# Kernel optimization log

Measured on AMD Instinct MI355X. Metric: run time of the kernel, lower is better.

Reference implementation:

```python
import jax, jax.numpy as jnp
import numpy as np
import math

B, T, E, H = 4, 2048, 1024, 16
D = E // H

def setup_inputs() -> dict:
    key = jax.random.key(0)
    k1, k2, k3 = jax.random.split(key, 3)
    x = jax.random.normal(k1, (B, T, E), dtype=jnp.float32)
    # GPT-2 Conv1D: out = x @ W + b, W shape [in, out]
    W_attn = jax.random.normal(k2, (E, 3 * E), dtype=jnp.float32) * 0.02
    b_attn = jnp.zeros((3 * E,), dtype=jnp.float32)
    W_proj = jax.random.normal(k3, (E, E), dtype=jnp.float32) * 0.02
    b_proj = jnp.zeros((E,), dtype=jnp.float32)
    # causal mask, broadcastable [1,1,T,T]; masked where mask == 0
    mask = jnp.tril(jnp.ones((T, T), dtype=jnp.int32))[None, None]
    return {"x": x, "mask": mask, "W_attn": W_attn, "b_attn": b_attn,
            "W_proj": W_proj, "b_proj": b_proj}

def reference(x, mask, W_attn, b_attn, W_proj, b_proj):
    Bx, Tx, Ex = x.shape
    qkv = x @ W_attn + b_attn                      # [B,T,3E]
    q, k, v = jnp.split(qkv, 3, axis=-1)
    q = q.reshape(Bx, Tx, H, D)
    k = k.reshape(Bx, Tx, H, D)
    v = v.reshape(Bx, Tx, H, D)
    att = jnp.einsum('bqhd,bkhd->bhqk', q, k) / math.sqrt(D)
    att = jnp.where(mask == 0, jnp.float32(-1e20), att)
    att = jax.nn.softmax(att, axis=-1)
    y = jnp.einsum('bhqk,bkhd->bqhd', att, v).reshape(Bx, Tx, Ex)
    y = y @ W_proj + b_proj
    return y
```

## Files before the change

### kernel.cpp

```cpp
#include <hip/hip_runtime.h>
#include <hip/hip_bf16.h>

#define BB 4
#define TT 2048
#define EE 1024
#define HH 16
#define DD 64
#define PART_SZ (BB*HH*TT*DD)

typedef __bf16 bf16x8_t __attribute__((ext_vector_type(8)));
typedef float floatx4_t __attribute__((ext_vector_type(4)));

__device__ __forceinline__ unsigned short f2bf(float f) {
    union { float f; unsigned int i; } v; v.f = f;
    unsigned int x = v.i;
    return (unsigned short)((x + 0x7FFFu + ((x >> 16) & 1u)) >> 16);
}
__device__ __forceinline__ unsigned int pack2(float lo, float hi) {
    return (unsigned int)f2bf(lo) | ((unsigned int)f2bf(hi) << 16);
}
__device__ __forceinline__ unsigned int cvt_pk_bf16(float lo, float hi) {
    unsigned int r;
    asm("v_cvt_pk_bf16_f32 %0, %1, %2" : "=v"(r) : "v"(lo), "v"(hi));
    return r;
}

typedef __attribute__((address_space(1))) const unsigned int gu32_t;
typedef __attribute__((address_space(3))) unsigned int lu32_t;
__device__ __forceinline__ void gl_lds16(const unsigned short* g, unsigned short* l) {
    __builtin_amdgcn_global_load_lds((gu32_t*)g, (lu32_t*)l, 16, 0, 0);
}

__global__ __launch_bounds__(256)
void cvt_x_k(const float* __restrict__ x, unsigned short* __restrict__ xb)
{
    const size_t i = ((size_t)blockIdx.x * 256 + threadIdx.x) * 8;
    float4 a = *(const float4*)(x + i);
    float4 b = *(const float4*)(x + i + 4);
    uint4 p;
    p.x = pack2(a.x, a.y); p.y = pack2(a.z, a.w);
    p.z = pack2(b.x, b.y); p.w = pack2(b.z, b.w);
    *(uint4*)(xb + i) = p;
}

__global__ __launch_bounds__(256)
void transpose_w_k(const float* __restrict__ W, unsigned short* __restrict__ WT, int N)
{
    __shared__ unsigned short L[64 * 72];
    const int tid = threadIdx.x;
    const int tn = blockIdx.x * 64;
    const int tk = blockIdx.y * 64;
    {
        const int k  = tid >> 2;
        const int n0 = (tid & 3) * 16;
        const float* src = W + (size_t)(tk + k) * N + tn + n0;
        float4 f0 = *(const float4*)(src);
        float4 f1 = *(const float4*)(src + 4);
        float4 f2 = *(const float4*)(src + 8);
        float4 f3 = *(const float4*)(src + 12);
        uint4 p0, p1;
        p0.x = pack2(f0.x, f0.y); p0.y = pack2(f0.z, f0.w);
        p0.z = pack2(f1.x, f1.y); p0.w = pack2(f1.z, f1.w);
        p1.x = pack2(f2.x, f2.y); p1.y = pack2(f2.z, f2.w);
        p1.z = pack2(f3.x, f3.y); p1.w = pack2(f3.z, f3.w);
        *(uint4*)(&L[k * 72 + n0])     = p0;
        *(uint4*)(&L[k * 72 + n0 + 8]) = p1;
    }
    __syncthreads();
    {
        const int n  = tid >> 2;
        const int k0 = (tid & 3) * 16;
        unsigned short u[16];
        #pragma unroll
        for (int e = 0; e < 16; e++) u[e] = L[(k0 + e) * 72 + n];
        unsigned short* dst = WT + (size_t)(tn + n) * 1024 + tk + k0;
        *(uint4*)(dst)     = *(uint4*)&u[0];
        *(uint4*)(dst + 8) = *(uint4*)&u[8];
    }
}

template<int MODE>
__global__ __launch_bounds__(256, 2)
void gemm_k(const unsigned short* __restrict__ Ag,
            const unsigned short* __restrict__ Wt,
            const float* __restrict__ biasg,
            unsigned short* __restrict__ Qo,
            unsigned short* __restrict__ Ko,
            unsigned short* __restrict__ Vo,
            float* __restrict__ Fo)
{
    constexpr int N = (MODE == 0) ? 3072 : 1024;
    __shared__ unsigned short Al[128 * 32];
    __shared__ unsigned short Bl[128 * 32];
    constexpr size_t EPSZ = (MODE == 0) ? (4 * 16 * 72 * 2) : (4 * 16 * 68 * 4);
    __shared__ __align__(16) char EpRaw[EPSZ];
    const int tid  = threadIdx.x;
    int bn, bm;
    if (MODE == 0) {
        const int id = blockIdx.x;
        const int s  = id & 7;
        const int t  = id >> 3;
        const int P  = (t / 12) * 8 + s;
        bm = (P >> 1) * 128;
        bn = ((P & 1) * 12 + (t % 12)) * 128;
    } else {
        const int id = blockIdx.x;
        const int s  = id & 7;
        const int t  = id >> 3;
        bm = ((t & 7) * 8 + s) * 128;
        bn = (t >> 3) * 128;
    }
    const int lane = tid & 63;
    const int wv   = tid >> 6;
    const int wm   = (wv & 1) * 64;
    const int wn   = (wv >> 1) * 64;
    const int l16  = lane & 15;
    const int quad = lane >> 4;
    const int lrow = lane >> 2;
    const int lk   = (lane & 3) * 8;

    const bool flip = (MODE == 1) || (bn < 2 * EE);

    floatx4_t acc[4][4];
    #pragma unroll
    for (int i = 0; i < 4; i++)
        #pragma unroll
        for (int j = 0; j < 4; j++)
            acc[i][j] = (floatx4_t){0.f, 0.f, 0.f, 0.f};

    for (int k0 = 0; k0 < 1024; k0 += 32) {
        __syncthreads();
        #pragma unroll
        for (int t = 0; t < 2; t++) {
            const int rb = wv * 32 + t * 16;
            gl_lds16(Ag + (size_t)(bm + rb + lrow) * 1024 + k0 + lk, &Al[rb * 32]);
            gl_lds16(Wt + (size_t)(bn + rb + lrow) * 1024 + k0 + lk, &Bl[rb * 32]);
        }
        __syncthreads();

        bf16x8_t af[4], bfr[4];
        #pragma unroll
        for (int i = 0; i < 4; i++)
            af[i]  = *(const bf16x8_t*)(&Al[(wm + i * 16 + l16) * 32 + quad * 8]);
        #pragma unroll
        for (int j = 0; j < 4; j++)
            bfr[j] = *(const bf16x8_t*)(&Bl[(wn + j * 16 + l16) * 32 + quad * 8]);
        if (flip) {
            #pragma unroll
            for (int u = 0; u < 4; u++)
                #pragma unroll
                for (int v = 0; v < 4; v++)
                    acc[u][v] = __builtin_amdgcn_mfma_f32_16x16x32_bf16(bfr[u], af[v], acc[u][v], 0, 0, 0);
        } else {
            #pragma unroll
            for (int u = 0; u < 4; u++)
                #pragma unroll
                for (int v = 0; v < 4; v++)
                    acc[u][v] = __builtin_amdgcn_mfma_f32_16x16x32_bf16(af[u], bfr[v], acc[u][v], 0, 0, 0);
        }
    }

    const int rdrow = lane >> 2;
    const int rdseg = (lane & 3) * 16;

    if (MODE == 1) {
        float* Epf = (float*)EpRaw + wv * 16 * 68;
        floatx4_t bv[4];
        #pragma unroll
        for (int u = 0; u < 4; u++)
            bv[u] = *(const floatx4_t*)(biasg + bn + wn + u * 16 + quad * 4);
        #pragma unroll
        for (int v = 0; v < 4; v++) {
            #pragma unroll
            for (int u = 0; u < 4; u++) {
                floatx4_t val;
                #pragma unroll
                for (int rr = 0; rr < 4; rr++) val[rr] = acc[u][v][rr] + bv[u][rr];
                *(floatx4_t*)(&Epf[l16 * 68 + u * 16 + quad * 4]) = val;
            }
            __builtin_amdgcn_s_waitcnt(0);
            const int m = bm + wm + v * 16 + rdrow;
            float* dst = Fo + (size_t)m * N + bn + wn + rdseg;
            const float* srcl = &Epf[rdrow * 68 + rdseg];
            #pragma unroll
            for (int c = 0; c < 4; c++)
                *(floatx4_t*)(dst + c * 4) = *(const floatx4_t*)(srcl + c * 4);
        }
    } else if (flip) {
        unsigned short* Ep = (unsigned short*)EpRaw + wv * 16 * 72;
        floatx4_t bv[4];
        #pragma unroll
        for (int u = 0; u < 4; u++)
            bv[u] = *(const floatx4_t*)(biasg + bn + wn + u * 16 + quad * 4);
        const int p  = bn >> 10;
        const int h  = ((bn + wn) & 1023) >> 6;
        const int d0 = rdseg & 63;
        unsigned short* outb = (p == 0) ? Qo : Ko;
        #pragma unroll
        for (int v = 0; v < 4; v++) {
            #pragma unroll
            for (int u = 0; u < 4; u++) {
                uint2 pk;
                pk.x = pack2(acc[u][v][0] + bv[u][0], acc[u][v][1] + bv[u][1]);
                pk.y = pack2(acc[u][v][2] + bv[u][2], acc[u][v][3] + bv[u][3]);
                *(uint2*)(&Ep[l16 * 72 + u * 16 + quad * 4]) = pk;
            }
            __builtin_amdgcn_s_waitcnt(0);
            const int t  = bm + wm + v * 16 + rdrow;
            const int b_ = t >> 11, t_ = t & 2047;
            unsigned short* dst = outb + ((size_t)(b_ * HH + h) * TT + t_) * DD + d0;
            const unsigned short* srcl = &Ep[rdrow * 72 + rdseg];
            *(uint4*)(dst)     = *(const uint4*)(srcl);
            *(uint4*)(dst + 8) = *(const uint4*)(srcl + 8);
        }
    } else {
        unsigned short* Ep = (unsigned short*)EpRaw + wv * 16 * 72;
        #pragma unroll
        for (int v = 0; v < 4; v++) {
            const float bias_v = biasg[bn + wn + v * 16 + l16];
            #pragma unroll
            for (int u = 0; u < 4; u++) {
                uint2 pk;
                pk.x = pack2(acc[u][v][0] + bias_v, acc[u][v][1] + bias_v);
                pk.y = pack2(acc[u][v][2] + bias_v, acc[u][v][3] + bias_v);
                *(uint2*)(&Ep[l16 * 72 + u * 16 + quad * 4]) = pk;
            }
            __builtin_amdgcn_s_waitcnt(0);
            const int n  = bn + wn + v * 16 + rdrow;
            const int h  = (n & 1023) >> 6, d = n & 63;
            const int t0 = bm + wm + rdseg;
            const int b_ = t0 >> 11, t_ = t0 & 2047;
            unsigned short* dst = Vo + ((size_t)(b_ * HH + h) * DD + d) * TT + t_;
            const unsigned short* srcl = &Ep[rdrow * 72 + rdseg];
            *(uint4*)(dst)     = *(const uint4*)(srcl);
            *(uint4*)(dst + 8) = *(const uint4*)(srcl + 8);
        }
    }
}

__global__ __launch_bounds__(256, 4)
void attn_k(const unsigned short* __restrict__ Qg,
            const unsigned short* __restrict__ Kg,
            const unsigned short* __restrict__ Vg,
            unsigned short* __restrict__ Og)
{
    __shared__ unsigned short Kt[64 * 72];
    __shared__ unsigned short Vt[64 * 72];
    __shared__ unsigned short Pw[4][16 * 72];
    const int tid  = threadIdx.x;
    const int w    = tid >> 6;
    const int lane = tid & 63;
    const int l16  = lane & 15;
    const int quad = lane >> 4;
    const int id = blockIdx.x;
    const int qt = 31 - ((id >> 3) & 31);
    const int bh = (id & 7) + 8 * (id >> 8);
    const int qb   = qt * 64;
    const int qw   = qb + w * 16;
    const size_t base = (size_t)bh * TT * DD;
    const float C = 0.18033688f;

    bf16x8_t qf[2];
    #pragma unroll
    for (int ks = 0; ks < 2; ks++)
        qf[ks] = *(const bf16x8_t*)(Qg + base + (size_t)(qw + l16) * DD + ks * 32 + quad * 8);

    floatx4_t oacc[4];
    #pragma unroll
    for (int n = 0; n < 4; n++) oacc[n] = (floatx4_t){0.f, 0.f, 0.f, 0.f};
    float lacc = 0.f;

    const int kend = qb + 64;
    const int srow = tid >> 2;
    const int sc0  = (tid & 3) * 16;
    const int qq   = qw + l16;
    const int kqb  = quad * 4;
    for (int kb = 0; kb < kend; kb += 64) {
        __syncthreads();
        {
            const unsigned short* kg = Kg + base + (size_t)(kb + srow) * DD + sc0;
            uint4 ka = *(const uint4*)(kg);
            uint4 kb2 = *(const uint4*)(kg + 8);
            *(uint4*)(&Kt[srow * 72 + sc0])     = ka;
            *(uint4*)(&Kt[srow * 72 + sc0 + 8]) = kb2;
            const unsigned short* vg = Vg + base + (size_t)srow * TT + kb + sc0;
            uint4 va = *(const uint4*)(vg);
            uint4 vb = *(const uint4*)(vg + 8);
            *(uint4*)(&Vt[srow * 72 + sc0])     = va;
            *(uint4*)(&Vt[srow * 72 + sc0 + 8]) = vb;
        }
        __syncthreads();
        if (kb < qw + 16) {
            floatx4_t sacc[4];
            #pragma unroll
            for (int n = 0; n < 4; n++) sacc[n] = (floatx4_t){0.f, 0.f, 0.f, 0.f};
            #pragma unroll
            for (int n = 0; n < 4; n++) {
                #pragma unroll
                for (int ks = 0; ks < 2; ks++) {
                    bf16x8_t kf = *(const bf16x8_t*)(&Kt[(n * 16 + l16) * 72 + ks * 32 + quad * 8]);
                    sacc[n] = __builtin_amdgcn_mfma_f32_16x16x32_bf16(kf, qf[ks], sacc[n], 0, 0, 0);
                }
            }
            if ((kb + 63) > qw) {
                #pragma unroll
                for (int n = 0; n < 4; n++) {
                    const int keyb = kb + n * 16 + kqb;
                    #pragma unroll
                    for (int rr = 0; rr < 4; rr++)
                        if (keyb + rr > qq) sacc[n][rr] = -1e30f;
                }
            }
            #pragma unroll
            for (int n = 0; n < 4; n++) {
                const float p0 = __builtin_exp2f(sacc[n][0] * C);
                const float p1 = __builtin_exp2f(sacc[n][1] * C);
                const float p2 = __builtin_exp2f(sacc[n][2] * C);
                const float p3 = __builtin_exp2f(sacc[n][3] * C);
                lacc += (p0 + p1) + (p2 + p3);
                uint2 pk;
                pk.x = cvt_pk_bf16(p0, p1);
                pk.y = cvt_pk_bf16(p2, p3);
                *(uint2*)(&Pw[w][l16 * 72 + n * 16 + kqb]) = pk;
            }
            bf16x8_t pf[2];
            #pragma unroll
            for (int ks = 0; ks < 2; ks++)
                pf[ks] = *(const bf16x8_t*)(&Pw[w][l16 * 72 + ks * 32 + quad * 8]);
            #pragma unroll
            for (int n = 0; n < 4; n++) {
                #pragma unroll
                for (int ks = 0; ks < 2; ks++) {
                    bf16x8_t vf = *(const bf16x8_t*)(&Vt[(n * 16 + l16) * 72 + ks * 32 + quad * 8]);
                    oacc[n] = __builtin_amdgcn_mfma_f32_16x16x32_bf16(pf[ks], vf, oacc[n], 0, 0, 0);
                }
            }
        }
    }
    float lsum = lacc;
    lsum += __shfl_xor(lsum, 16);
    lsum += __shfl_xor(lsum, 32);
    const float inv = 1.f / lsum;
    const int b_ = bh >> 4, h_ = bh & 15;
    #pragma unroll
    for (int rr = 0; rr < 4; rr++) {
        const float invr = __int_as_float(
            __builtin_amdgcn_ds_bpermute((quad * 4 + rr) * 4, __float_as_int(inv)));
        const int q = qw + quad * 4 + rr;
        unsigned short* op = Og + (((size_t)b_ * TT + q) * HH + h_) * DD;
        #pragma unroll
        for (int n = 0; n < 4; n++)
            op[n * 16 + l16] = f2bf(oacc[n][rr] * invr);
    }
}

extern "C" void kernel_launch(void* const* d_in, const int* in_sizes, int n_in,
                              void* d_out, int out_size, void* d_ws, size_t ws_size,
                              hipStream_t stream) {
    const float* x      = (const float*)d_in[0];
    const float* W_attn = (const float*)d_in[2];
    const float* b_attn = (const float*)d_in[3];
    const float* W_proj = (const float*)d_in[4];
    const float* b_proj = (const float*)d_in[5];
    float* out = (float*)d_out;

    unsigned short* Qs  = (unsigned short*)d_out;
    unsigned short* Ks  = Qs + (size_t)PART_SZ;
    unsigned short* VTs = (unsigned short*)d_ws;
    unsigned short* Ao  = VTs + (size_t)PART_SZ;
    unsigned short* Xb  = Ao + (size_t)PART_SZ;
    unsigned short* WaT = Xb + (size_t)PART_SZ;
    unsigned short* WpT = WaT + (size_t)3072 * 1024;

    cvt_x_k<<<PART_SZ / (256 * 8), 256, 0, stream>>>(x, Xb);
    transpose_w_k<<<dim3(48, 16), 256, 0, stream>>>(W_attn, WaT, 3072);
    transpose_w_k<<<dim3(16, 16), 256, 0, stream>>>(W_proj, WpT, 1024);

    gemm_k<0><<<1536, 256, 0, stream>>>(Xb, WaT, b_attn, Qs, Ks, VTs, nullptr);

    attn_k<<<2048, 256, 0, stream>>>(Qs, Ks, VTs, Ao);

    gemm_k<1><<<512, 256, 0, stream>>>(Ao, WpT, b_proj, nullptr, nullptr, nullptr, out);
}
```

Baseline: 305.2 us.

## Pair causal query tiles per block to share K/V loads; prescale Q

Measured after the change: 287.0 us. -6.0%, faster.

```diff
diff --git a/kernel.cpp b/kernel.cpp
--- a/kernel.cpp
+++ b/kernel.cpp
@@ -196,13 +196,14 @@
         const int h  = ((bn + wn) & 1023) >> 6;
         const int d0 = rdseg & 63;
         unsigned short* outb = (p == 0) ? Qo : Ko;
+        const float sc = (p == 0) ? 0.18033688f : 1.0f;
         #pragma unroll
         for (int v = 0; v < 4; v++) {
             #pragma unroll
             for (int u = 0; u < 4; u++) {
                 uint2 pk;
-                pk.x = pack2(acc[u][v][0] + bv[u][0], acc[u][v][1] + bv[u][1]);
-                pk.y = pack2(acc[u][v][2] + bv[u][2], acc[u][v][3] + bv[u][3]);
+                pk.x = pack2((acc[u][v][0] + bv[u][0]) * sc, (acc[u][v][1] + bv[u][1]) * sc);
+                pk.y = pack2((acc[u][v][2] + bv[u][2]) * sc, (acc[u][v][3] + bv[u][3]) * sc);
                 *(uint2*)(&Ep[l16 * 72 + u * 16 + quad * 4]) = pk;
             }
             __builtin_amdgcn_s_waitcnt(0);
@@ -253,28 +254,86 @@
     const int l16  = lane & 15;
     const int quad = lane >> 4;
     const int id = blockIdx.x;
-    const int qt = 31 - ((id >> 3) & 31);
-    const int bh = (id & 7) + 8 * (id >> 8);
-    const int qb   = qt * 64;
-    const int qw   = qb + w * 16;
+    const int J  = (id >> 3) & 15;
+    const int bh = (id & 7) + 8 * (id >> 7);
+    const int qb0 = J * 64;
+    const int qb1 = (31 - J) * 64;
+    const int qw0 = qb0 + w * 16;
+    const int qw1 = qb1 + w * 16;
     const size_t base = (size_t)bh * TT * DD;
-    const float C = 0.18033688f;
-
-    bf16x8_t qf[2];
+
+    bf16x8_t qf0[2], qf1[2];
     #pragma unroll
-    for (int ks = 0; ks < 2; ks++)
-        qf[ks] = *(const bf16x8_t*)(Qg + base + (size_t)(qw + l16) * DD + ks * 32 + quad * 8);
-
-    floatx4_t oacc[4];
+    for (int ks = 0; ks < 2; ks++) {
+        qf0[ks] = *(const bf16x8_t*)(Qg + base + (size_t)(qw0 + l16) * DD + ks * 32 + quad * 8);
+        qf1[ks] = *(const bf16x8_t*)(Qg + base + (size_t)(qw1 + l16) * DD + ks * 32 + quad * 8);
+    }
+
+    floatx4_t oacc0[4], oacc1[4];
     #pragma unroll
-    for (int n = 0; n < 4; n++) oacc[n] = (floatx4_t){0.f, 0.f, 0.f, 0.f};
-    float lacc = 0.f;
-
-    const int kend = qb + 64;
+    for (int n = 0; n < 4; n++) {
+        oacc0[n] = (floatx4_t){0.f, 0.f, 0.f, 0.f};
+        oacc1[n] = (floatx4_t){0.f, 0.f, 0.f, 0.f};
+    }
+    float lacc0 = 0.f, lacc1 = 0.f;
+
+    const int kend = qb1 + 64;
     const int srow = tid >> 2;
     const int sc0  = (tid & 3) * 16;
-    const int qq   = qw + l16;
     const int kqb  = quad * 4;
+    const int qq0  = qw0 + l16;
+    const int qq1  = qw1 + l16;
+
+    auto COMP = [&](int kb, int qw, int qq, const bf16x8_t* qf,
+                    floatx4_t* oacc, float& lacc) {
+        if (kb < qw + 16) {
+            floatx4_t sacc[4];
+            #pragma unroll
+            for (int n = 0; n < 4; n++) sacc[n] = (floatx4_t){0.f, 0.f, 0.f, 0.f};
+            #pragma unroll
+            for (int n = 0; n < 4; n++) {
+                #pragma unroll
+                for (int ks = 0; ks < 2; ks++) {
+                    bf16x8_t kf = *(const bf16x8_t*)(&Kt[(n * 16 + l16) * 72 + ks * 32 + quad * 8]);
+                    sacc[n] = __builtin_amdgcn_mfma_f32_16x16x32_bf16(kf, qf[ks], sacc[n], 0, 0, 0);
+                }
+            }
+            if ((kb + 63) > qw) {
+                #pragma unroll
+                for (int n = 0; n < 4; n++) {
+                    const int keyb = kb + n * 16 + kqb;
+                    #pragma unroll
+                    for (int rr = 0; rr < 4; rr++)
+                        if (keyb + rr > qq) sacc[n][rr] = -1e30f;
+                }
+            }
+            #pragma unroll
+            for (int n = 0; n < 4; n++) {
+                const float p0 = __builtin_exp2f(sacc[n][0]);
+                const float p1 = __builtin_exp2f(sacc[n][1]);
+                const float p2 = __builtin_exp2f(sacc[n][2]);
+                const float p3 = __builtin_exp2f(sacc[n][3]);
+                lacc += (p0 + p1) + (p2 + p3);
+                uint2 pk;
+                pk.x = cvt_pk_bf16(p0, p1);
+                pk.y = cvt_pk_bf16(p2, p3);
+                *(uint2*)(&Pw[w][l16 * 72 + n * 16 + kqb]) = pk;
+            }
+            bf16x8_t pf[2];
+            #pragma unroll
+            for (int ks = 0; ks < 2; ks++)
+                pf[ks] = *(const bf16x8_t*)(&Pw[w][l16 * 72 + ks * 32 + quad * 8]);
+            #pragma unroll
+            for (int n = 0; n < 4; n++) {
+                #pragma unroll
+                for (int ks = 0; ks < 2; ks++) {
+                    bf16x8_t vf = *(const bf16x8_t*)(&Vt[(n * 16 + l16) * 72 + ks * 32 + quad * 8]);
+                    oacc[n] = __builtin_amdgcn_mfma_f32_16x16x32_bf16(pf[ks], vf, oacc[n], 0, 0, 0);
+                }
+            }
+        }
+    };
+
     for (int kb = 0; kb < kend; kb += 64) {
         __syncthreads();
         {
@@ -290,68 +349,29 @@
             *(uint4*)(&Vt[srow * 72 + sc0 + 8]) = vb;
         }
         __syncthreads();
-        if (kb < qw + 16) {
-            floatx4_t sacc[4];
-            #pragma unroll
-            for (int n = 0; n < 4; n++) sacc[n] = (floatx4_t){0.f, 0.f, 0.f, 0.f};
-            #pragma unroll
-            for (int n = 0; n < 4; n++) {
-                #pragma unroll
-                for (int ks = 0; ks < 2; ks++) {
-                    bf16x8_t kf = *(const bf16x8_t*)(&Kt[(n * 16 + l16) * 72 + ks * 32 + quad * 8]);
-                    sacc[n] = __builtin_amdgcn_mfma_f32_16x16x32_bf16(kf, qf[ks], sacc[n], 0, 0, 0);
-                }
-            }
-            if ((kb + 63) > qw) {
-                #pragma unroll
-                for (int n = 0; n < 4; n++) {
-                    const int keyb = kb + n * 16 + kqb;
-                    #pragma unroll
-                    for (int rr = 0; rr < 4; rr++)
-                        if (keyb + rr > qq) sacc[n][rr] = -1e30f;
-                }
-            }
-            #pragma unroll
-            for (int n = 0; n < 4; n++) {
-                const float p0 = __builtin_exp2f(sacc[n][0] * C);
-                const float p1 = __builtin_exp2f(sacc[n][1] * C);
-                const float p2 = __builtin_exp2f(sacc[n][2] * C);
-                const float p3 = __builtin_exp2f(sacc[n][3] * C);
-                lacc += (p0 + p1) + (p2 + p3);
-                uint2 pk;
-                pk.x = cvt_pk_bf16(p0, p1);
-                pk.y = cvt_pk_bf16(p2, p3);
-                *(uint2*)(&Pw[w][l16 * 72 + n * 16 + kqb]) = pk;
-            }
-            bf16x8_t pf[2];
-            #pragma unroll
-            for (int ks = 0; ks < 2; ks++)
-                pf[ks] = *(const bf16x8_t*)(&Pw[w][l16 * 72 + ks * 32 + quad * 8]);
-            #pragma unroll
-            for (int n = 0; n < 4; n++) {
-                #pragma unroll
-                for (int ks = 0; ks < 2; ks++) {
-                    bf16x8_t vf = *(const bf16x8_t*)(&Vt[(n * 16 + l16) * 72 + ks * 32 + quad * 8]);
-                    oacc[n] = __builtin_amdgcn_mfma_f32_16x16x32_bf16(pf[ks], vf, oacc[n], 0, 0, 0);
-                }
-            }
-        }
-    }
-    float lsum = lacc;
-    lsum += __shfl_xor(lsum, 16);
-    lsum += __shfl_xor(lsum, 32);
-    const float inv = 1.f / lsum;
+        COMP(kb, qw0, qq0, qf0, oacc0, lacc0);
+        COMP(kb, qw1, qq1, qf1, oacc1, lacc1);
+    }
+
     const int b_ = bh >> 4, h_ = bh & 15;
-    #pragma unroll
-    for (int rr = 0; rr < 4; rr++) {
-        const float invr = __int_as_float(
-            __builtin_amdgcn_ds_bpermute((quad * 4 + rr) * 4, __float_as_int(inv)));
-        const int q = qw + quad * 4 + rr;
-        unsigned short* op = Og + (((size_t)b_ * TT + q) * HH + h_) * DD;
-        #pragma unroll
-        for (int n = 0; n < 4; n++)
-            op[n * 16 + l16] = f2bf(oacc[n][rr] * invr);
-    }
+    auto EPI = [&](int qw, float lacc, const floatx4_t* oacc) {
+        float lsum = lacc;
+        lsum += __shfl_xor(lsum, 16);
+        lsum += __shfl_xor(lsum, 32);
+        const float inv = 1.f / lsum;
+        #pragma unroll
+        for (int rr = 0; rr < 4; rr++) {
+            const float invr = __int_as_float(
+                __builtin_amdgcn_ds_bpermute((quad * 4 + rr) * 4, __float_as_int(inv)));
+            const int q = qw + quad * 4 + rr;
+            unsigned short* op = Og + (((size_t)b_ * TT + q) * HH + h_) * DD;
+            #pragma unroll
+            for (int n = 0; n < 4; n++)
+                op[n * 16 + l16] = f2bf(oacc[n][rr] * invr);
+        }
+    };
+    EPI(qw0, lacc0, oacc0);
+    EPI(qw1, lacc1, oacc1);
 }
 
 extern "C" void kernel_launch(void* const* d_in, const int* in_sizes, int n_in,
@@ -378,7 +398,7 @@
 
     gemm_k<0><<<1536, 256, 0, stream>>>(Xb, WaT, b_attn, Qs, Ks, VTs, nullptr);
 
-    attn_k<<<2048, 256, 0, stream>>>(Qs, Ks, VTs, Ao);
+    attn_k<<<1024, 256, 0, stream>>>(Qs, Ks, VTs, Ao);
 
     gemm_k<1><<<512, 256, 0, stream>>>(Ao, WpT, b_proj, nullptr, nullptr, nullptr, out);
 }
```
